# Kernel optimization log

Hardware: AMD Instinct MI355X
Metric: run time of the kernel (lower is better)

Reference implementation:

```python
import jax, jax.numpy as jnp
import numpy as np

B, CE, CD = 4, 128, 256
HE = WE = 256
HD = WD = 128
N = CE // 8  # 16


def _up2_align_corners(x):
    # bilinear upsample x2 with align_corners=True (matches nn.UpsamplingBilinear2d)
    def axis_up(x, axis, n_in):
        n_out = 2 * n_in
        pos = jnp.arange(n_out, dtype=x.dtype) * ((n_in - 1) / (n_out - 1))
        i0 = jnp.clip(jnp.floor(pos).astype(jnp.int32), 0, n_in - 1)
        i1 = jnp.clip(i0 + 1, 0, n_in - 1)
        w = pos - i0.astype(x.dtype)
        shape = [1] * x.ndim
        shape[axis] = n_out
        w = w.reshape(shape)
        return jnp.take(x, i0, axis=axis) * (1 - w) + jnp.take(x, i1, axis=axis) * w
    x = axis_up(x, 2, x.shape[2])
    return axis_up(x, 3, x.shape[3])


def _conv7(x, w, b):
    y = jax.lax.conv_general_dilated(x, w, (1, 1), [(3, 3), (3, 3)],
                                     dimension_numbers=('NCHW', 'OIHW', 'NCHW'))
    return y + b.reshape(1, -1, 1, 1)


def _sag_branch(x, w1, b1, w2, b2):
    mx = jnp.max(x, axis=1, keepdims=True)           # channel max-pool [B,1,H,W]
    av = jnp.mean(x, axis=1, keepdims=True)          # channel avg-pool
    c1 = jnp.einsum('bchw,oc->bohw', x, w1) + b1.reshape(1, -1, 1, 1)  # 1x1 conv -> 1 ch
    return _conv7(jnp.concatenate([mx, av, c1], axis=1), w2, b2)       # [B,1,H,W]


def _cag_branch(x, wa, ba, wm, bm):
    av = jnp.mean(x, axis=(2, 3))                    # [B,C] global avg
    mx = jnp.max(x, axis=(2, 3))                     # [B,C] global max
    return av @ wa.T + ba + mx @ wm.T + bm           # [B,N]


def setup_inputs() -> dict:
    key = jax.random.key(0)
    ks = jax.random.split(key, 20)
    s = 0.02
    return {
        'x_enc': jax.random.normal(ks[0], (B, CE, HE, WE), jnp.float32),
        'x_dec': jax.random.normal(ks[1], (B, CD, HD, WD), jnp.float32),
        'cw_ea': jax.random.normal(ks[2], (N, CE), jnp.float32) * s,
        'cb_ea': jnp.zeros((N,), jnp.float32),
        'cw_em': jax.random.normal(ks[3], (N, CE), jnp.float32) * s,
        'cb_em': jnp.zeros((N,), jnp.float32),
        'cw_da': jax.random.normal(ks[4], (N, CD), jnp.float32) * s,
        'cb_da': jnp.zeros((N,), jnp.float32),
        'cw_dm': jax.random.normal(ks[5], (N, CD), jnp.float32) * s,
        'cb_dm': jnp.zeros((N,), jnp.float32),
        'cw_f': jax.random.normal(ks[6], (CE, N), jnp.float32) * s,
        'cb_f': jnp.zeros((CE,), jnp.float32),
        'sw1_e': jax.random.normal(ks[7], (1, CE), jnp.float32) * s,
        'sb1_e': jnp.zeros((1,), jnp.float32),
        'sw2_e': jax.random.normal(ks[8], (1, 3, 7, 7), jnp.float32) * s,
        'sb2_e': jnp.zeros((1,), jnp.float32),
        'sw1_d': jax.random.normal(ks[9], (1, CD), jnp.float32) * s,
        'sb1_d': jnp.zeros((1,), jnp.float32),
        'sw2_d': jax.random.normal(ks[10], (1, 3, 7, 7), jnp.float32) * s,
        'sb2_d': jnp.zeros((1,), jnp.float32),
        'save_attention': 0,
    }


def reference(x_enc, x_dec, cw_ea, cb_ea, cw_em, cb_em, cw_da, cb_da, cw_dm, cb_dm,
              cw_f, cb_f, sw1_e, sb1_e, sw2_e, sb2_e, sw1_d, sb1_d, sw2_d, sb2_d,
              save_attention):
    # decoder path: upsample x2 (align_corners=True) + ReLU
    dec_feat = jax.nn.relu(_up2_align_corners(x_dec))  # [B,CD,2HD,2WD]
    # encoder path: center crop to match
    h2, w2 = 2 * x_dec.shape[2], 2 * x_dec.shape[3]
    s0 = (x_enc.shape[2] - h2) // 2
    s1 = (x_enc.shape[3] - w2) // 2
    enc_feat = x_enc[:, :, s0:s0 + h2, s1:s1 + w2]
    # spatial attention gate (sAG)
    spat = jax.nn.sigmoid(_sag_branch(enc_feat, sw1_e, sb1_e, sw2_e, sb2_e)
                          + _sag_branch(dec_feat, sw1_d, sb1_d, sw2_d, sb2_d))  # [B,1,H,W]
    # channel attention gate (cAG)
    ce = _cag_branch(enc_feat, cw_ea, cb_ea, cw_em, cb_em)  # [B,N]
    cd = _cag_branch(dec_feat, cw_da, cb_da, cw_dm, cb_dm)  # [B,N]
    ch = jax.nn.sigmoid((ce + cd) @ cw_f.T + cb_f)           # [B,CE]
    return enc_feat * spat * ch[:, :, None, None]
```

## Files before the change

### kernel.cpp

```cpp
#include <hip/hip_runtime.h>
#include <math.h>

static const int B_  = 4;
static const int CE_ = 128;
static const int CD_ = 256;
static const int HE_ = 256;
static const int HD_ = 128;
static const int N_  = 16;
#define PLANE  65536
#define DPLANE 16384
#define UPSCALE (127.0f/255.0f)

__device__ __forceinline__ float4 fmax4(float4 a, float4 b) {
  return make_float4(fmaxf(a.x, b.x), fmaxf(a.y, b.y), fmaxf(a.z, b.z), fmaxf(a.w, b.w));
}
__device__ __forceinline__ float4 fadd4(float4 a, float4 b) {
  return make_float4(a.x + b.x, a.y + b.y, a.z + b.z, a.w + b.w);
}

__global__ __launch_bounds__(256) void k_stats(
    const float* __restrict__ xe, const float* __restrict__ xd,
    const float* __restrict__ sw1e, const float* __restrict__ sb1e,
    const float* __restrict__ sw1d, const float* __restrict__ sb1d,
    float* __restrict__ stats, float* __restrict__ eav, float* __restrict__ emx,
    float* __restrict__ dav, float* __restrict__ dmx) {
  __shared__ float smem[1024];
  __shared__ float4 red[3][256];
  int blk = blockIdx.x;
  int t = threadIdx.x;

  if (blk < 1024) {
    int b = blk >> 8, h = blk & 255;
    int cs = t >> 6, q = t & 63;
    float bias = sb1e[0];
    if (t < CE_) smem[t] = sw1e[t];
    __syncthreads();
    const float4* base = (const float4*)xe + (size_t)b * CE_ * (PLANE / 4)
                         + (size_t)h * 64 + q;
    float4 mx4 = make_float4(-INFINITY, -INFINITY, -INFINITY, -INFINITY);
    float4 sm4 = make_float4(0.f, 0.f, 0.f, 0.f);
    float4 pj4 = make_float4(0.f, 0.f, 0.f, 0.f);
#pragma unroll 4
    for (int c = cs; c < CE_; c += 4) {
      float4 v = base[(size_t)c * (PLANE / 4)];
      float wc = smem[c];
      mx4 = fmax4(mx4, v);
      sm4 = fadd4(sm4, v);
      pj4.x = fmaf(v.x, wc, pj4.x); pj4.y = fmaf(v.y, wc, pj4.y);
      pj4.z = fmaf(v.z, wc, pj4.z); pj4.w = fmaf(v.w, wc, pj4.w);
    }
    red[0][t] = mx4; red[1][t] = sm4; red[2][t] = pj4;
    __syncthreads();
    if (t < 64) {
      float4 m = fmax4(fmax4(red[0][t], red[0][t + 64]),
                       fmax4(red[0][t + 128], red[0][t + 192]));
      float4 s = fadd4(fadd4(red[1][t], red[1][t + 64]),
                       fadd4(red[1][t + 128], red[1][t + 192]));
      float4 p = fadd4(fadd4(red[2][t], red[2][t + 64]),
                       fadd4(red[2][t + 128], red[2][t + 192]));
      float4* so = (float4*)stats;
      size_t o4 = (size_t)(b * 6) * (PLANE / 4) + (size_t)h * 64 + t;
      so[o4] = m;
      s.x *= (1.f / CE_); s.y *= (1.f / CE_); s.z *= (1.f / CE_); s.w *= (1.f / CE_);
      so[o4 + PLANE / 4] = s;
      p.x += bias; p.y += bias; p.z += bias; p.w += bias;
      so[o4 + 2 * (PLANE / 4)] = p;
    }

  } else if (blk < 1536) {
    int bc = blk - 1024;
    const float4* p = (const float4*)(xe + (size_t)bc * PLANE);
    float sm = 0.f, m = -INFINITY;
    for (int i = t; i < PLANE / 4; i += 256) {
      float4 v = p[i];
      sm += (v.x + v.y) + (v.z + v.w);
      m = fmaxf(m, fmaxf(fmaxf(v.x, v.y), fmaxf(v.z, v.w)));
    }
    float* ss = smem;
    float* sx = smem + 256;
    ss[t] = sm; sx[t] = m;
    __syncthreads();
    for (int s = 128; s > 0; s >>= 1) {
      if (t < s) { ss[t] += ss[t + s]; sx[t] = fmaxf(sx[t], sx[t + s]); }
      __syncthreads();
    }
    if (t == 0) { eav[bc] = ss[0] * (1.f / PLANE); emx[bc] = sx[0]; }

  } else if (blk < 2560) {
    int bh = blk - 1536;
    int b = bh >> 8, h = bh & 255;
    float bias = sb1d[0];
    float* swt  = smem;
    float* buf0 = smem + 256;
    float* buf1 = smem + 512;
    swt[t] = sw1d[t];
    float ph = (float)h * UPSCALE;
    int ih0 = (int)ph; float wh = ph - (float)ih0;
    int ih1 = min(ih0 + 1, HD_ - 1);
    int rowoff = (ih1 - ih0) * HD_;
    float pw = (float)t * UPSCALE;
    int iw0 = (int)pw; float ww = pw - (float)iw0;
    int iw1 = min(iw0 + 1, HD_ - 1);
    const float* xb = xd + (size_t)b * CD_ * DPLANE + ih0 * HD_;
    int li = min(t, DPLANE - ih0 * HD_ - 1);
    float pre = xb[li];
    float mx = -INFINITY, sm = 0.f, pj = 0.f;
    for (int c = 0; c < CD_; ++c) {
      float* bw = (c & 1) ? buf1 : buf0;
      bw[t] = pre;
      if (c + 1 < CD_) pre = xb[(size_t)(c + 1) * DPLANE + li];
      __syncthreads();
      float l00 = bw[iw0], l01 = bw[iw1];
      float l10 = bw[rowoff + iw0], l11 = bw[rowoff + iw1];
      float top = l00 + ww * (l01 - l00);
      float bot = l10 + ww * (l11 - l10);
      float v = fmaxf(top + wh * (bot - top), 0.f);
      mx = fmaxf(mx, v);
      sm += v;
      pj = fmaf(v, swt[c], pj);
    }
    size_t o = (((size_t)b * 6 + 3) * HE_ + h) * (size_t)HE_ + t;
    stats[o] = mx;
    stats[o + (size_t)PLANE] = sm * (1.f / CD_);
    stats[o + 2 * (size_t)PLANE] = pj + bias;

  } else {
    int bc = blk - 2560;
    const float* p = xd + (size_t)bc * DPLANE;
    int*   so0  = (int*)smem;
    int*   so1  = so0 + 256;
    float* swht = smem + 512;
    {
      float ph = (float)t * UPSCALE;
      int ih0 = (int)ph;
      so0[t]  = ih0 * HD_;
      so1[t]  = min(ih0 + 1, HD_ - 1) * HD_;
      swht[t] = ph - (float)ih0;
    }
    float pw = (float)t * UPSCALE;
    int iw0 = (int)pw; float ww = pw - (float)iw0;
    int iw1 = min(iw0 + 1, HD_ - 1);
    __syncthreads();
    float sm = 0.f, m = -INFINITY;
#pragma unroll 4
    for (int hh = 0; hh < 256; ++hh) {
      const float* r0 = p + so0[hh];
      const float* r1 = p + so1[hh];
      float wh = swht[hh];
      float top = r0[iw0] * (1.f - ww) + r0[iw1] * ww;
      float bot = r1[iw0] * (1.f - ww) + r1[iw1] * ww;
      float v = fmaxf((1.f - wh) * top + wh * bot, 0.f);
      sm += v;
      m = fmaxf(m, v);
    }
    __syncthreads();
    float* ss = smem;
    float* sx = smem + 256;
    ss[t] = sm; sx[t] = m;
    __syncthreads();
    for (int s = 128; s > 0; s >>= 1) {
      if (t < s) { ss[t] += ss[t + s]; sx[t] = fmaxf(sx[t], sx[t + s]); }
      __syncthreads();
    }
    if (t == 0) { dav[bc] = ss[0] * (1.f / PLANE); dmx[bc] = sx[0]; }
  }
}

__global__ __launch_bounds__(256) void k_gate(
    const float* __restrict__ stats,
    const float* __restrict__ we, const float* __restrict__ be,
    const float* __restrict__ wd, const float* __restrict__ bd,
    const float* __restrict__ eav, const float* __restrict__ emx,
    const float* __restrict__ dav, const float* __restrict__ dmx,
    const float* __restrict__ cw_ea, const float* __restrict__ cb_ea,
    const float* __restrict__ cw_em, const float* __restrict__ cb_em,
    const float* __restrict__ cw_da, const float* __restrict__ cb_da,
    const float* __restrict__ cw_dm, const float* __restrict__ cb_dm,
    const float* __restrict__ cw_f, const float* __restrict__ cb_f,
    const float* __restrict__ x, float* __restrict__ out) {
  int bh = blockIdx.x;
  int b = bh >> 8, h = bh & 255;
  int t = threadIdx.x;
  int w = t;

  __shared__ float swE[147], swD[147];
  __shared__ float part[16][17];
  __shared__ float s_n[16];
  __shared__ float s_ch[128];
  __shared__ float s_spat[256];

  if (t < 147) { swE[t] = we[t]; swD[t] = wd[t]; }

  {
    int n = t & 15, sl = t >> 4;
    const float* ea = eav + b * CE_;
    const float* em = emx + b * CE_;
    const float* da = dav + b * CD_;
    const float* dm = dmx + b * CD_;
    float p = 0.f;
#pragma unroll
    for (int i = 0; i < 8; ++i) {
      int c = sl * 8 + i;
      p = fmaf(ea[c], cw_ea[n * CE_ + c], p);
      p = fmaf(em[c], cw_em[n * CE_ + c], p);
    }
#pragma unroll
    for (int i = 0; i < 16; ++i) {
      int c = sl * 16 + i;
      p = fmaf(da[c], cw_da[n * CD_ + c], p);
      p = fmaf(dm[c], cw_dm[n * CD_ + c], p);
    }
    part[n][sl] = p;
  }
  __syncthreads();
  if (t < 16) {
    float s = cb_ea[t] + cb_em[t] + cb_da[t] + cb_dm[t];
#pragma unroll
    for (int sl = 0; sl < 16; ++sl) s += part[t][sl];
    s_n[t] = s;
  }
  __syncthreads();
  if (t < 128) {
    float s = cb_f[t];
#pragma unroll
    for (int n = 0; n < N_; ++n) s = fmaf(s_n[n], cw_f[t * N_ + n], s);
    s_ch[t] = 1.f / (1.f + __expf(-s));
  }

  float acc = be[0] + bd[0];
  const float* sb = stats + ((size_t)b * 6) * PLANE;
#pragma unroll
  for (int ic = 0; ic < 3; ++ic) {
    const float* pe = sb + (size_t)ic * PLANE;
    const float* pd = sb + (size_t)(ic + 3) * PLANE;
#pragma unroll
    for (int ky = 0; ky < 7; ++ky) {
      int y = h + ky - 3;
      if ((unsigned)y >= 256u) continue;
      const float* rowE = pe + y * 256;
      const float* rowD = pd + y * 256;
#pragma unroll
      for (int kx = 0; kx < 7; ++kx) {
        int xw = w + kx - 3;
        if ((unsigned)xw >= 256u) continue;
        float we_ = swE[ic * 49 + ky * 7 + kx];
        float wd_ = swD[ic * 49 + ky * 7 + kx];
        acc = fmaf(rowE[xw], we_, acc);
        acc = fmaf(rowD[xw], wd_, acc);
      }
    }
  }
  s_spat[w] = 1.f / (1.f + __expf(-acc));
  __syncthreads();

  int w4 = t & 63;
  int cq = t >> 6;
  float4 sv = ((const float4*)s_spat)[w4];
  const float4* xp = (const float4*)x + ((size_t)b * CE_) * (PLANE / 4) + h * 64;
  float4*       op = (float4*)out     + ((size_t)b * CE_) * (PLANE / 4) + h * 64;
  for (int c = cq; c < CE_; c += 4) {
    float cv = s_ch[c];
    float4 xv = xp[(size_t)c * (PLANE / 4) + w4];
    float4 o;
    o.x = xv.x * sv.x * cv;
    o.y = xv.y * sv.y * cv;
    o.z = xv.z * sv.z * cv;
    o.w = xv.w * sv.w * cv;
    op[(size_t)c * (PLANE / 4) + w4] = o;
  }
}

extern "C" void kernel_launch(void* const* d_in, const int* in_sizes, int n_in,
                              void* d_out, int out_size, void* d_ws, size_t ws_size,
                              hipStream_t stream) {
  const float* x_enc = (const float*)d_in[0];
  const float* x_dec = (const float*)d_in[1];
  const float* cw_ea = (const float*)d_in[2];
  const float* cb_ea = (const float*)d_in[3];
  const float* cw_em = (const float*)d_in[4];
  const float* cb_em = (const float*)d_in[5];
  const float* cw_da = (const float*)d_in[6];
  const float* cb_da = (const float*)d_in[7];
  const float* cw_dm = (const float*)d_in[8];
  const float* cb_dm = (const float*)d_in[9];
  const float* cw_f  = (const float*)d_in[10];
  const float* cb_f  = (const float*)d_in[11];
  const float* sw1_e = (const float*)d_in[12];
  const float* sb1_e = (const float*)d_in[13];
  const float* sw2_e = (const float*)d_in[14];
  const float* sb2_e = (const float*)d_in[15];
  const float* sw1_d = (const float*)d_in[16];
  const float* sb1_d = (const float*)d_in[17];
  const float* sw2_d = (const float*)d_in[18];
  const float* sb2_d = (const float*)d_in[19];
  float* out = (float*)d_out;
  (void)in_sizes; (void)n_in; (void)out_size; (void)ws_size;

  float* ws    = (float*)d_ws;
  float* stats = ws;
  float* eav   = ws + 1572864;
  float* emx   = eav + 512;
  float* dav   = emx + 512;
  float* dmx   = dav + 1024;

  k_stats<<<3584, 256, 0, stream>>>(x_enc, x_dec, sw1_e, sb1_e, sw1_d, sb1_d,
                                    stats, eav, emx, dav, dmx);
  k_gate <<<B_ * HE_, 256, 0, stream>>>(stats, sw2_e, sb2_e, sw2_d, sb2_d,
                                        eav, emx, dav, dmx,
                                        cw_ea, cb_ea, cw_em, cb_em,
                                        cw_da, cb_da, cw_dm, cb_dm,
                                        cw_f, cb_f, x_enc, out);
}
```

Measured before the change: 438.7 us.

## Reorder stats blocks, batch decoder channels four per barrier, stage plane in LDS

```diff
diff --git a/kernel.cpp b/kernel.cpp
--- a/kernel.cpp
+++ b/kernel.cpp
@@ -24,75 +24,16 @@
     const float* __restrict__ sw1d, const float* __restrict__ sb1d,
     float* __restrict__ stats, float* __restrict__ eav, float* __restrict__ emx,
     float* __restrict__ dav, float* __restrict__ dmx) {
-  __shared__ float smem[1024];
-  __shared__ float4 red[3][256];
+  __shared__ float smem[4864];
   int blk = blockIdx.x;
   int t = threadIdx.x;
 
   if (blk < 1024) {
     int b = blk >> 8, h = blk & 255;
-    int cs = t >> 6, q = t & 63;
-    float bias = sb1e[0];
-    if (t < CE_) smem[t] = sw1e[t];
-    __syncthreads();
-    const float4* base = (const float4*)xe + (size_t)b * CE_ * (PLANE / 4)
-                         + (size_t)h * 64 + q;
-    float4 mx4 = make_float4(-INFINITY, -INFINITY, -INFINITY, -INFINITY);
-    float4 sm4 = make_float4(0.f, 0.f, 0.f, 0.f);
-    float4 pj4 = make_float4(0.f, 0.f, 0.f, 0.f);
-#pragma unroll 4
-    for (int c = cs; c < CE_; c += 4) {
-      float4 v = base[(size_t)c * (PLANE / 4)];
-      float wc = smem[c];
-      mx4 = fmax4(mx4, v);
-      sm4 = fadd4(sm4, v);
-      pj4.x = fmaf(v.x, wc, pj4.x); pj4.y = fmaf(v.y, wc, pj4.y);
-      pj4.z = fmaf(v.z, wc, pj4.z); pj4.w = fmaf(v.w, wc, pj4.w);
-    }
-    red[0][t] = mx4; red[1][t] = sm4; red[2][t] = pj4;
-    __syncthreads();
-    if (t < 64) {
-      float4 m = fmax4(fmax4(red[0][t], red[0][t + 64]),
-                       fmax4(red[0][t + 128], red[0][t + 192]));
-      float4 s = fadd4(fadd4(red[1][t], red[1][t + 64]),
-                       fadd4(red[1][t + 128], red[1][t + 192]));
-      float4 p = fadd4(fadd4(red[2][t], red[2][t + 64]),
-                       fadd4(red[2][t + 128], red[2][t + 192]));
-      float4* so = (float4*)stats;
-      size_t o4 = (size_t)(b * 6) * (PLANE / 4) + (size_t)h * 64 + t;
-      so[o4] = m;
-      s.x *= (1.f / CE_); s.y *= (1.f / CE_); s.z *= (1.f / CE_); s.w *= (1.f / CE_);
-      so[o4 + PLANE / 4] = s;
-      p.x += bias; p.y += bias; p.z += bias; p.w += bias;
-      so[o4 + 2 * (PLANE / 4)] = p;
-    }
-
-  } else if (blk < 1536) {
-    int bc = blk - 1024;
-    const float4* p = (const float4*)(xe + (size_t)bc * PLANE);
-    float sm = 0.f, m = -INFINITY;
-    for (int i = t; i < PLANE / 4; i += 256) {
-      float4 v = p[i];
-      sm += (v.x + v.y) + (v.z + v.w);
-      m = fmaxf(m, fmaxf(fmaxf(v.x, v.y), fmaxf(v.z, v.w)));
-    }
-    float* ss = smem;
-    float* sx = smem + 256;
-    ss[t] = sm; sx[t] = m;
-    __syncthreads();
-    for (int s = 128; s > 0; s >>= 1) {
-      if (t < s) { ss[t] += ss[t + s]; sx[t] = fmaxf(sx[t], sx[t + s]); }
-      __syncthreads();
-    }
-    if (t == 0) { eav[bc] = ss[0] * (1.f / PLANE); emx[bc] = sx[0]; }
-
-  } else if (blk < 2560) {
-    int bh = blk - 1536;
-    int b = bh >> 8, h = bh & 255;
     float bias = sb1d[0];
     float* swt  = smem;
-    float* buf0 = smem + 256;
-    float* buf1 = smem + 512;
+    float* bufA = smem + 256;
+    float* bufB = smem + 1280;
     swt[t] = sw1d[t];
     float ph = (float)h * UPSCALE;
     int ih0 = (int)ph; float wh = ph - (float)ih0;
@@ -103,57 +44,89 @@
     int iw1 = min(iw0 + 1, HD_ - 1);
     const float* xb = xd + (size_t)b * CD_ * DPLANE + ih0 * HD_;
     int li = min(t, DPLANE - ih0 * HD_ - 1);
-    float pre = xb[li];
+    float pre0 = xb[li];
+    float pre1 = xb[DPLANE + li];
+    float pre2 = xb[2 * DPLANE + li];
+    float pre3 = xb[3 * DPLANE + li];
     float mx = -INFINITY, sm = 0.f, pj = 0.f;
-    for (int c = 0; c < CD_; ++c) {
-      float* bw = (c & 1) ? buf1 : buf0;
-      bw[t] = pre;
-      if (c + 1 < CD_) pre = xb[(size_t)(c + 1) * DPLANE + li];
-      __syncthreads();
-      float l00 = bw[iw0], l01 = bw[iw1];
-      float l10 = bw[rowoff + iw0], l11 = bw[rowoff + iw1];
-      float top = l00 + ww * (l01 - l00);
-      float bot = l10 + ww * (l11 - l10);
-      float v = fmaxf(top + wh * (bot - top), 0.f);
-      mx = fmaxf(mx, v);
-      sm += v;
-      pj = fmaf(v, swt[c], pj);
+    for (int p = 0; p < 64; ++p) {
+      float* bw = (p & 1) ? bufB : bufA;
+      bw[t] = pre0; bw[256 + t] = pre1; bw[512 + t] = pre2; bw[768 + t] = pre3;
+      if (p + 1 < 64) {
+        const float* nx = xb + (size_t)(4 * (p + 1)) * DPLANE;
+        pre0 = nx[li];
+        pre1 = nx[DPLANE + li];
+        pre2 = nx[2 * DPLANE + li];
+        pre3 = nx[3 * DPLANE + li];
+      }
+      __syncthreads();
+#pragma unroll
+      for (int j = 0; j < 4; ++j) {
+        const float* bb = bw + j * 256;
+        float l00 = bb[iw0], l01 = bb[iw1];
+        float l10 = bb[rowoff + iw0], l11 = bb[rowoff + iw1];
+        float top = l00 + ww * (l01 - l00);
+        float bot = l10 + ww * (l11 - l10);
+        float v = fmaxf(top + wh * (bot - top), 0.f);
+        mx = fmaxf(mx, v);
+        sm += v;
+        pj = fmaf(v, swt[4 * p + j], pj);
+      }
     }
     size_t o = (((size_t)b * 6 + 3) * HE_ + h) * (size_t)HE_ + t;
     stats[o] = mx;
     stats[o + (size_t)PLANE] = sm * (1.f / CD_);
     stats[o + 2 * (size_t)PLANE] = pj + bias;
 
-  } else {
-    int bc = blk - 2560;
-    const float* p = xd + (size_t)bc * DPLANE;
-    int*   so0  = (int*)smem;
-    int*   so1  = so0 + 256;
-    float* swht = smem + 512;
-    {
-      float ph = (float)t * UPSCALE;
-      int ih0 = (int)ph;
-      so0[t]  = ih0 * HD_;
-      so1[t]  = min(ih0 + 1, HD_ - 1) * HD_;
-      swht[t] = ph - (float)ih0;
-    }
+  } else if (blk < 2048) {
+    int bc = blk - 1024;
+    const float* plane = xd + (size_t)bc * DPLANE;
+    float* stage = smem;
+    float* ss = smem + 4352;
+    float* sx = smem + 4608;
     float pw = (float)t * UPSCALE;
     int iw0 = (int)pw; float ww = pw - (float)iw0;
     int iw1 = min(iw0 + 1, HD_ - 1);
-    __syncthreads();
     float sm = 0.f, m = -INFINITY;
+    for (int k = 0; k < 4; ++k) {
+      int w0   = (k == 0) ? 0 : (32 * k - 1);
+      int rend = (k == 3) ? 128 : (32 * (k + 1) + 1);
+      int nf = (rend - w0) * HD_;
+      __syncthreads();
+      for (int idx = t; idx < nf; idx += 256) stage[idx] = plane[w0 * HD_ + idx];
+      __syncthreads();
+      int h0 = 64 * k;
 #pragma unroll 4
-    for (int hh = 0; hh < 256; ++hh) {
-      const float* r0 = p + so0[hh];
-      const float* r1 = p + so1[hh];
-      float wh = swht[hh];
-      float top = r0[iw0] * (1.f - ww) + r0[iw1] * ww;
-      float bot = r1[iw0] * (1.f - ww) + r1[iw1] * ww;
-      float v = fmaxf((1.f - wh) * top + wh * bot, 0.f);
-      sm += v;
-      m = fmaxf(m, v);
-    }
-    __syncthreads();
+      for (int hh = h0; hh < h0 + 64; ++hh) {
+        float ph = (float)hh * UPSCALE;
+        int ih0 = (int)ph; float wh = ph - (float)ih0;
+        int r0 = (ih0 - w0) * HD_;
+        int r1 = (min(ih0 + 1, HD_ - 1) - w0) * HD_;
+        float top = stage[r0 + iw0] * (1.f - ww) + stage[r0 + iw1] * ww;
+        float bot = stage[r1 + iw0] * (1.f - ww) + stage[r1 + iw1] * ww;
+        float v = fmaxf((1.f - wh) * top + wh * bot, 0.f);
+        sm += v;
+        m = fmaxf(m, v);
+      }
+    }
+    __syncthreads();
+    ss[t] = sm; sx[t] = m;
+    __syncthreads();
+    for (int s = 128; s > 0; s >>= 1) {
+      if (t < s) { ss[t] += ss[t + s]; sx[t] = fmaxf(sx[t], sx[t + s]); }
+      __syncthreads();
+    }
+    if (t == 0) { dav[bc] = ss[0] * (1.f / PLANE); dmx[bc] = sx[0]; }
+
+  } else if (blk < 2560) {
+    int bc = blk - 2048;
+    const float4* p = (const float4*)(xe + (size_t)bc * PLANE);
+    float sm = 0.f, m = -INFINITY;
+    for (int i = t; i < PLANE / 4; i += 256) {
+      float4 v = p[i];
+      sm += (v.x + v.y) + (v.z + v.w);
+      m = fmaxf(m, fmaxf(fmaxf(v.x, v.y), fmaxf(v.z, v.w)));
+    }
     float* ss = smem;
     float* sx = smem + 256;
     ss[t] = sm; sx[t] = m;
@@ -162,7 +135,48 @@
       if (t < s) { ss[t] += ss[t + s]; sx[t] = fmaxf(sx[t], sx[t + s]); }
       __syncthreads();
     }
-    if (t == 0) { dav[bc] = ss[0] * (1.f / PLANE); dmx[bc] = sx[0]; }
+    if (t == 0) { eav[bc] = ss[0] * (1.f / PLANE); emx[bc] = sx[0]; }
+
+  } else {
+    int bh = blk - 2560;
+    int b = bh >> 8, h = bh & 255;
+    int cs = t >> 6, q = t & 63;
+    float bias = sb1e[0];
+    float*  wt  = smem;
+    float4* red = (float4*)(smem + 128);
+    if (t < CE_) wt[t] = sw1e[t];
+    __syncthreads();
+    const float4* base = (const float4*)xe + (size_t)b * CE_ * (PLANE / 4)
+                         + (size_t)h * 64 + q;
+    float4 mx4 = make_float4(-INFINITY, -INFINITY, -INFINITY, -INFINITY);
+    float4 sm4 = make_float4(0.f, 0.f, 0.f, 0.f);
+    float4 pj4 = make_float4(0.f, 0.f, 0.f, 0.f);
+#pragma unroll 4
+    for (int c = cs; c < CE_; c += 4) {
+      float4 v = base[(size_t)c * (PLANE / 4)];
+      float wc = wt[c];
+      mx4 = fmax4(mx4, v);
+      sm4 = fadd4(sm4, v);
+      pj4.x = fmaf(v.x, wc, pj4.x); pj4.y = fmaf(v.y, wc, pj4.y);
+      pj4.z = fmaf(v.z, wc, pj4.z); pj4.w = fmaf(v.w, wc, pj4.w);
+    }
+    red[t] = mx4; red[256 + t] = sm4; red[512 + t] = pj4;
+    __syncthreads();
+    if (t < 64) {
+      float4 m = fmax4(fmax4(red[t], red[t + 64]),
+                       fmax4(red[t + 128], red[t + 192]));
+      float4 s = fadd4(fadd4(red[256 + t], red[256 + t + 64]),
+                       fadd4(red[256 + t + 128], red[256 + t + 192]));
+      float4 p = fadd4(fadd4(red[512 + t], red[512 + t + 64]),
+                       fadd4(red[512 + t + 128], red[512 + t + 192]));
+      float4* so = (float4*)stats;
+      size_t o4 = (size_t)(b * 6) * (PLANE / 4) + (size_t)h * 64 + t;
+      so[o4] = m;
+      s.x *= (1.f / CE_); s.y *= (1.f / CE_); s.z *= (1.f / CE_); s.w *= (1.f / CE_);
+      so[o4 + PLANE / 4] = s;
+      p.x += bias; p.y += bias; p.z += bias; p.w += bias;
+      so[o4 + 2 * (PLANE / 4)] = p;
+    }
   }
 }
 
```

Result: faster. 407.3 us (-7.2%).
